# Kernel tuning notes

Hardware: AMD Instinct MI355X
Metric: run time of the kernel (lower is better)

The kernel has to match this reference:

```python
import jax, jax.numpy as jnp
import numpy as np

B, N, D = 2, 2048, 1024
H = 16
D_HEAD = D // H
WINDOW = 128


def setup_inputs() -> dict:
    key = jax.random.key(0)
    ks = jax.random.split(key, 9)
    s = 1.0 / np.sqrt(D)
    return {
        "x": jax.random.normal(ks[0], (B, N, D), dtype=jnp.float32),
        "Wq": jax.random.uniform(ks[1], (D, D), jnp.float32, -s, s),
        "bq": jax.random.uniform(ks[2], (D,), jnp.float32, -s, s),
        "Wk": jax.random.uniform(ks[3], (D, D), jnp.float32, -s, s),
        "bk": jax.random.uniform(ks[4], (D,), jnp.float32, -s, s),
        "Wv": jax.random.uniform(ks[5], (D, D), jnp.float32, -s, s),
        "bv": jax.random.uniform(ks[6], (D,), jnp.float32, -s, s),
        "Wo": jax.random.uniform(ks[7], (D, D), jnp.float32, -s, s),
        "bo": jax.random.uniform(ks[8], (D,), jnp.float32, -s, s),
    }


def reference(x, Wq, bq, Wk, bk, Wv, bv, Wo, bo):
    # Projections (torch Linear: x @ W.T + b), split into heads: (B,H,N,d)
    def proj(W, b):
        y = x @ W.T + b
        return y.reshape(B, N, H, D_HEAD).transpose(0, 2, 1, 3)

    Q = proj(Wq, bq)
    K = proj(Wk, bk)
    V = proj(Wv, bv)

    scale = 1.0 / np.sqrt(D_HEAD)
    scores = jnp.einsum("bhqd,bhkd->bhqk", Q, K) * scale  # (B,H,N,N)

    i = jnp.arange(N)[:, None]
    j = jnp.arange(N)[None, :]
    band = jnp.abs(i - j) <= WINDOW  # (N,N) sliding-window band mask
    scores = jnp.where(band, scores, -jnp.inf)

    probs = jax.nn.softmax(scores, axis=-1)
    out = jnp.einsum("bhqk,bhkd->bhqd", probs, V)  # (B,H,N,d)
    out = out.transpose(0, 2, 1, 3).reshape(B, N, D)
    return out @ Wo.T + bo
```

## Files before the change

kernel.cpp:

```cpp
#include <hip/hip_runtime.h>
#include <hip/hip_bf16.h>
#include <stdint.h>

typedef __bf16 bf16_t;
typedef __bf16 bf16x8 __attribute__((ext_vector_type(8)));
typedef float f32x4 __attribute__((ext_vector_type(4)));

#define NB 2
#define NN 2048
#define ND 1024
#define NH 16
#define DHEAD 64
#define WIN 128

__device__ __forceinline__ void load_lds16(const void* g, void* l) {
  __builtin_amdgcn_global_load_lds(
      (const __attribute__((address_space(1))) uint32_t*)g,
      (__attribute__((address_space(3))) uint32_t*)l, 16, 0, 0);
}

__global__ __launch_bounds__(256)
void cast_all(const float* __restrict__ x,
              const float* __restrict__ Wq, const float* __restrict__ Wk,
              const float* __restrict__ Wv, const float* __restrict__ Wo,
              bf16_t* __restrict__ xb,
              bf16_t* __restrict__ Wqb, bf16_t* __restrict__ Wkb,
              bf16_t* __restrict__ Wvb, bf16_t* __restrict__ Wob) {
  int i = blockIdx.x * 256 + threadIdx.x;
  const float* in;
  bf16_t* out;
  int off;
  if (i < 1048576) {
    in = x; out = xb; off = i;
  } else {
    int j = i - 1048576;
    int wsel = j >> 18;
    off = j & 262143;
    in  = (wsel == 0) ? Wq  : (wsel == 1) ? Wk  : (wsel == 2) ? Wv  : Wo;
    out = (wsel == 0) ? Wqb : (wsel == 1) ? Wkb : (wsel == 2) ? Wvb : Wob;
  }
  float4 v = reinterpret_cast<const float4*>(in)[off];
  union { bf16_t h[4]; uint2 u; } o;
  o.h[0] = (bf16_t)v.x; o.h[1] = (bf16_t)v.y;
  o.h[2] = (bf16_t)v.z; o.h[3] = (bf16_t)v.w;
  reinterpret_cast<uint2*>(out)[off] = o.u;
}

__global__ __launch_bounds__(512, 6)
void qkv_gemm(const bf16_t* __restrict__ xb,
              const bf16_t* __restrict__ Wqb, const bf16_t* __restrict__ Wkb,
              const bf16_t* __restrict__ Wvb,
              const float* __restrict__ bq, const float* __restrict__ bk,
              const float* __restrict__ bv,
              bf16_t* __restrict__ Qh, bf16_t* __restrict__ Kh,
              bf16_t* __restrict__ VTt) {
  __shared__ __align__(16) bf16_t As[2 * 4096];
  __shared__ __align__(16) bf16_t Bs[2 * 4096];

  const int z = blockIdx.z;
  const bf16_t* Bw  = (z == 0) ? Wqb : (z == 1) ? Wkb : Wvb;
  const float* bias = (z == 0) ? bq  : (z == 1) ? bk  : bv;
  const int m0 = blockIdx.y * 128, n0 = blockIdx.x * 128;

  const int tid = threadIdx.x, lane = tid & 63, w = tid >> 6;
  const int wm = w >> 2, wn = w & 3;
  const int lrow = lane & 15, lkg = lane >> 4;
  const int sr = lane >> 2;
  const int sc = ((lane & 3) ^ ((lane >> 3) & 3)) * 8;

  const bf16_t* abase = xb + (size_t)(m0 + w * 16 + sr) * 1024 + sc;
  const bf16_t* bbase = Bw + (size_t)(n0 + w * 16 + sr) * 1024 + sc;

  f32x4 acc[4][2] = {};

  auto stage = [&](int buf, int k0) {
    load_lds16(abase + k0, As + buf * 4096 + w * 512);
    load_lds16(bbase + k0, Bs + buf * 4096 + w * 512);
  };

  stage(0, 0);
  __syncthreads();

  for (int t = 0; t < 32; ++t) {
    if (t < 31) stage((t + 1) & 1, (t + 1) << 5);
    const bf16_t* Ab = As + (t & 1) * 4096;
    const bf16_t* Bb = Bs + (t & 1) * 4096;
    bf16x8 af[4], bf[2];
#pragma unroll
    for (int m = 0; m < 4; ++m) {
      const int row = wm * 64 + m * 16 + lrow;
      af[m] = *reinterpret_cast<const bf16x8*>(Ab + row * 32 + ((lkg ^ ((row >> 1) & 3)) << 3));
    }
#pragma unroll
    for (int n = 0; n < 2; ++n) {
      const int row = wn * 32 + n * 16 + lrow;
      bf[n] = *reinterpret_cast<const bf16x8*>(Bb + row * 32 + ((lkg ^ ((row >> 1) & 3)) << 3));
    }
#pragma unroll
    for (int m = 0; m < 4; ++m)
#pragma unroll
      for (int n = 0; n < 2; ++n)
        acc[m][n] = __builtin_amdgcn_mfma_f32_16x16x32_bf16(af[m], bf[n], acc[m][n], 0, 0, 0);
    __syncthreads();
  }

#pragma unroll
  for (int m = 0; m < 4; ++m)
#pragma unroll
    for (int n = 0; n < 2; ++n)
#pragma unroll
      for (int r = 0; r < 4; ++r) {
        int row = m0 + wm * 64 + m * 16 + lkg * 4 + r;
        int col = n0 + wn * 32 + n * 16 + lrow;
        float val = acc[m][n][r] + bias[col];
        int bb = row >> 11, tok = row & 2047;
        int hh = col >> 6,  dd = col & 63;
        if (z == 2) {
          VTt[((((size_t)(bb * NH + hh) * 32 + (tok >> 6)) * 64 + dd) << 6) + (tok & 63)] = (bf16_t)val;
        } else {
          bf16_t* outp = (z == 0) ? Qh : Kh;
          outp[(((size_t)(bb * NH + hh) * NN + tok) << 6) + dd] = (bf16_t)val;
        }
      }
}

__global__ __launch_bounds__(512, 2)
void out_gemm3(const bf16_t* __restrict__ AOb, const bf16_t* __restrict__ Wob,
               const float* __restrict__ bo, float* __restrict__ Cout) {
  __shared__ __align__(16) bf16_t lds[24576];

  const int m0 = blockIdx.y * 128, n0 = blockIdx.x * 64;
  const int tid = threadIdx.x, lane = tid & 63, w = tid >> 6;
  const int g = w >> 2;
  const int pr = w & 3;
  const int wr = pr >> 1, wc = pr & 1;
  const int lrow = lane & 15, lkg = lane >> 4;
  const int sr = lane >> 2;
  const int sc = ((lane & 3) ^ ((lane >> 3) & 3)) * 8;

  const bf16_t* abase = AOb + (size_t)(m0 + sr) * 1024 + g * 512 + sc;
  const bf16_t* bbase = Wob + (size_t)(n0 + pr * 16 + sr) * 1024 + g * 512 + sc;

  f32x4 acc[4][2] = {};

  auto stage = [&](int buf, int k0) {
    bf16_t* seg = &lds[(g * 2 + buf) * 6144];
#pragma unroll
    for (int i = 0; i < 2; ++i) {
      const int unit = pr * 2 + i;
      load_lds16(abase + (size_t)unit * 16 * 1024 + k0, seg + unit * 512);
    }
    load_lds16(bbase + k0, seg + 4096 + pr * 512);
  };

  stage(0, 0);
  __syncthreads();

  for (int t = 0; t < 16; ++t) {
    if (t < 15) stage((t + 1) & 1, (t + 1) << 5);
    const bf16_t* seg = &lds[(g * 2 + (t & 1)) * 6144];
    const bf16_t* Bb = seg + 4096;
    bf16x8 af[4], bf[2];
#pragma unroll
    for (int m = 0; m < 4; ++m) {
      const int row = wr * 64 + m * 16 + lrow;
      af[m] = *reinterpret_cast<const bf16x8*>(seg + row * 32 + ((lkg ^ ((row >> 1) & 3)) << 3));
    }
#pragma unroll
    for (int n = 0; n < 2; ++n) {
      const int row = wc * 32 + n * 16 + lrow;
      bf[n] = *reinterpret_cast<const bf16x8*>(Bb + row * 32 + ((lkg ^ ((row >> 1) & 3)) << 3));
    }
#pragma unroll
    for (int m = 0; m < 4; ++m)
#pragma unroll
      for (int n = 0; n < 2; ++n)
        acc[m][n] = __builtin_amdgcn_mfma_f32_16x16x32_bf16(af[m], bf[n], acc[m][n], 0, 0, 0);
    __syncthreads();
  }

  float* fl = reinterpret_cast<float*>(lds);
  if (g == 1) {
#pragma unroll
    for (int m = 0; m < 4; ++m)
#pragma unroll
      for (int n = 0; n < 2; ++n)
#pragma unroll
        for (int r = 0; r < 4; ++r)
          fl[pr * 2048 + ((m * 2 + n) * 4 + r) * 64 + lane] = acc[m][n][r];
  }
  __syncthreads();
  if (g == 0) {
#pragma unroll
    for (int m = 0; m < 4; ++m)
#pragma unroll
      for (int n = 0; n < 2; ++n)
#pragma unroll
        for (int r = 0; r < 4; ++r) {
          int row = m0 + wr * 64 + m * 16 + lkg * 4 + r;
          int col = n0 + wc * 32 + n * 16 + lrow;
          float val = acc[m][n][r] + fl[pr * 2048 + ((m * 2 + n) * 4 + r) * 64 + lane] + bo[col];
          Cout[(size_t)row * 1024 + col] = val;
        }
  }
}

__global__ __launch_bounds__(256)
void attn_kernel(const bf16_t* __restrict__ Qh, const bf16_t* __restrict__ Kh,
                 const bf16_t* __restrict__ VTt, bf16_t* __restrict__ AO) {
  __shared__ __align__(16) bf16_t KV_lds[2][2][4096];
  __shared__ uint32_t P_lds[4][16][32];

  const int work = ((blockIdx.x & 7) << 7) | (blockIdx.x >> 3);
  const int qt = work & 31, h = (work >> 5) & 15, b = work >> 9;
  const int tid = threadIdx.x, lane = tid & 63, w = tid >> 6;
  const int lrow = lane & 15, lkg = lane >> 4;
  const int q0 = qt * 64;
  const int qb = q0 + w * 16;
  const int qrow = qb + lrow;
  const int rs7 = lrow & 7;

  const int srow8 = lane >> 3;
  const int sswz  = 8 * ((lane & 7) ^ srow8);

  const bf16_t* kbase = Kh  + (((size_t)(b * NH + h) * NN) << 6);
  const bf16_t* vbase = VTt + ((size_t)(b * NH + h) * 32) * 4096;

  const bf16_t* qptr = Qh + (((size_t)(b * NH + h) * NN + qrow) << 6) + lkg * 8;
  bf16x8 qf0 = *reinterpret_cast<const bf16x8*>(qptr);
  bf16x8 qf1 = *reinterpret_cast<const bf16x8*>(qptr + 32);

  float m_run = -1e30f, l_run = 0.f;
  f32x4 o[4] = {};

  const int kstart = (q0 - WIN > 0) ? (q0 - WIN) : 0;
  const int kend = (q0 + 64 + WIN < NN) ? (q0 + 64 + WIN) : NN;
  const int nch = (kend - kstart) >> 6;
  const float scale = 0.125f;

  auto stage = [&](int bufi, int kc) {
#pragma unroll
    for (int j = 0; j < 2; ++j) {
      const int i = w * 2 + j;
      load_lds16(kbase + (((size_t)(kc + i * 8 + srow8)) << 6) + sswz,
                 &KV_lds[bufi][0][i * 512]);
      load_lds16(vbase + (((size_t)((kc >> 6) * 64 + i * 8 + srow8)) << 6) + sswz,
                 &KV_lds[bufi][1][i * 512]);
    }
  };

  stage(0, kstart);
  __syncthreads();

  for (int ic = 0; ic < nch; ++ic) {
    const int kc = kstart + ic * 64;
    const int bi = ic & 1;
    if (ic + 1 < nch) stage(bi ^ 1, kc + 64);

    const bf16_t* Kt = &KV_lds[bi][0][0];
    const bf16_t* Vt = &KV_lds[bi][1][0];

    f32x4 s[4];
#pragma unroll
    for (int t = 0; t < 4; ++t) {
      const bf16_t* kr = Kt + (t * 16 + lrow) * 64;
      bf16x8 kf0 = *reinterpret_cast<const bf16x8*>(kr + ((lkg ^ rs7) << 3));
      bf16x8 kf1 = *reinterpret_cast<const bf16x8*>(kr + (((4 + lkg) ^ rs7) << 3));
      f32x4 zz = {};
      zz = __builtin_amdgcn_mfma_f32_16x16x32_bf16(kf0, qf0, zz, 0, 0, 0);
      zz = __builtin_amdgcn_mfma_f32_16x16x32_bf16(kf1, qf1, zz, 0, 0, 0);
      s[t] = zz;
    }

    bf16x8 vf0[4], vf1[4];
#pragma unroll
    for (int f = 0; f < 4; ++f) {
      const bf16_t* vr = Vt + (f * 16 + lrow) * 64;
      vf0[f] = *reinterpret_cast<const bf16x8*>(vr + ((lkg ^ rs7) << 3));
      vf1[f] = *reinterpret_cast<const bf16x8*>(vr + (((4 + lkg) ^ rs7) << 3));
    }

    const bool needs_mask = (kc < qb - 113) || (kc > qb + 65);
    float p[4][4];
    float mloc = -1e30f, rsum = 0.f;
    if (needs_mask) {
      float v[4][4];
#pragma unroll
      for (int t = 0; t < 4; ++t)
#pragma unroll
        for (int r = 0; r < 4; ++r) {
          int k = kc + t * 16 + lkg * 4 + r;
          int d = qrow - k;
          bool ok = (unsigned)(d + WIN) <= 2u * WIN;
          v[t][r] = ok ? s[t][r] * scale : -1e30f;
          mloc = fmaxf(mloc, v[t][r]);
        }
      mloc = fmaxf(mloc, __shfl_xor(mloc, 16, 64));
      mloc = fmaxf(mloc, __shfl_xor(mloc, 32, 64));
      float mn = fmaxf(m_run, mloc);
      float corr = __expf(m_run - mn);
      m_run = mn;
#pragma unroll
      for (int t = 0; t < 4; ++t)
#pragma unroll
        for (int r = 0; r < 4; ++r) {
          int k = kc + t * 16 + lkg * 4 + r;
          int d = qrow - k;
          bool ok = (unsigned)(d + WIN) <= 2u * WIN;
          p[t][r] = ok ? __expf(v[t][r] - mn) : 0.f;
          rsum += p[t][r];
        }
      rsum += __shfl_xor(rsum, 16, 64);
      rsum += __shfl_xor(rsum, 32, 64);
      l_run = l_run * corr + rsum;
#pragma unroll
      for (int f = 0; f < 4; ++f) o[f] *= corr;
    } else {
      float v[4][4];
#pragma unroll
      for (int t = 0; t < 4; ++t)
#pragma unroll
        for (int r = 0; r < 4; ++r) {
          v[t][r] = s[t][r] * scale;
          mloc = fmaxf(mloc, v[t][r]);
        }
      mloc = fmaxf(mloc, __shfl_xor(mloc, 16, 64));
      mloc = fmaxf(mloc, __shfl_xor(mloc, 32, 64));
      float mn = fmaxf(m_run, mloc);
      float corr = __expf(m_run - mn);
      m_run = mn;
#pragma unroll
      for (int t = 0; t < 4; ++t)
#pragma unroll
        for (int r = 0; r < 4; ++r) {
          p[t][r] = __expf(v[t][r] - mn);
          rsum += p[t][r];
        }
      rsum += __shfl_xor(rsum, 16, 64);
      rsum += __shfl_xor(rsum, 32, 64);
      l_run = l_run * corr + rsum;
#pragma unroll
      for (int f = 0; f < 4; ++f) o[f] *= corr;
    }

    uint32_t* prow = &P_lds[w][lrow][0];
#pragma unroll
    for (int t = 0; t < 4; ++t)
#pragma unroll
      for (int c = 0; c < 2; ++c) {
        union { bf16_t hh[2]; uint32_t u; } pk;
        pk.hh[0] = (bf16_t)p[t][2 * c];
        pk.hh[1] = (bf16_t)p[t][2 * c + 1];
        int L = 8 * t + 2 * lkg + c;
        int pos = (((L >> 2) ^ rs7) << 2) | (L & 3);
        prow[pos] = pk.u;
      }
    asm volatile("" ::: "memory");
    const bf16_t* prd = reinterpret_cast<const bf16_t*>(&P_lds[w][lrow][0]);
    bf16x8 pa0 = *reinterpret_cast<const bf16x8*>(prd + ((lkg ^ rs7) << 3));
    bf16x8 pa1 = *reinterpret_cast<const bf16x8*>(prd + (((4 + lkg) ^ rs7) << 3));

#pragma unroll
    for (int f = 0; f < 4; ++f) {
      o[f] = __builtin_amdgcn_mfma_f32_16x16x32_bf16(vf0[f], pa0, o[f], 0, 0, 0);
      o[f] = __builtin_amdgcn_mfma_f32_16x16x32_bf16(vf1[f], pa1, o[f], 0, 0, 0);
    }
    __syncthreads();
  }

  float inv = 1.0f / l_run;
#pragma unroll
  for (int f = 0; f < 4; ++f) {
    union { bf16_t hh[4]; uint2 u; } ov;
#pragma unroll
    for (int r = 0; r < 4; ++r) ov.hh[r] = (bf16_t)(o[f][r] * inv);
    bf16_t* op = AO + (size_t)(b * NN + qrow) * ND + h * DHEAD + f * 16 + lkg * 4;
    *reinterpret_cast<uint2*>(op) = ov.u;
  }
}

extern "C" void kernel_launch(void* const* d_in, const int* in_sizes, int n_in,
                              void* d_out, int out_size, void* d_ws, size_t ws_size,
                              hipStream_t stream) {
  const float* x  = (const float*)d_in[0];
  const float* Wq = (const float*)d_in[1];
  const float* bq = (const float*)d_in[2];
  const float* Wk = (const float*)d_in[3];
  const float* bk = (const float*)d_in[4];
  const float* Wv = (const float*)d_in[5];
  const float* bv = (const float*)d_in[6];
  const float* Wo = (const float*)d_in[7];
  const float* bo = (const float*)d_in[8];
  float* out = (float*)d_out;

  bf16_t* ws  = (bf16_t*)d_ws;
  bf16_t* xb  = ws;
  bf16_t* Wqb = xb  + 4194304;
  bf16_t* Wkb = Wqb + 1048576;
  bf16_t* Wvb = Wkb + 1048576;
  bf16_t* Wob = Wvb + 1048576;
  bf16_t* Qh  = Wob + 1048576;
  bf16_t* Kh  = Qh  + 4194304;
  bf16_t* VTt = Kh  + 4194304;
  bf16_t* AOb = VTt + 4194304;

  cast_all<<<8192, 256, 0, stream>>>(x, Wq, Wk, Wv, Wo, xb, Wqb, Wkb, Wvb, Wob);

  qkv_gemm<<<dim3(8, 32, 3), 512, 0, stream>>>(xb, Wqb, Wkb, Wvb, bq, bk, bv, Qh, Kh, VTt);
  attn_kernel<<<1024, 256, 0, stream>>>(Qh, Kh, VTt, AOb);
  out_gemm3<<<dim3(16, 32), 512, 0, stream>>>(AOb, Wob, bo, out);
}
```

Measured before the change: 91.29 us.

## Enlarge QKV GEMM tiles to 256x256 with triple-buffered LDS pipeline

Reworks the QKV projection GEMM from 128x128 tiles with a double buffer to 256x256 tiles with a three-stage LDS ring. A and B loads for step t+2 are interleaved between two MFMA half-phases, using explicit waitcnt, barriers and setprio. The launch becomes a 1D grid of 192 blocks with a swizzled block-to-tile mapping to improve L2 reuse. Each thread carries more accumulators and occupancy drops to 2 waves per SIMD. With only 192 blocks on the device, some CUs may be left underused.

```diff
diff --git a/kernel.cpp b/kernel.cpp
--- a/kernel.cpp
+++ b/kernel.cpp
@@ -46,7 +46,7 @@
   reinterpret_cast<uint2*>(out)[off] = o.u;
 }
 
-__global__ __launch_bounds__(512, 6)
+__global__ __launch_bounds__(512, 2)
 void qkv_gemm(const bf16_t* __restrict__ xb,
               const bf16_t* __restrict__ Wqb, const bf16_t* __restrict__ Wkb,
               const bf16_t* __restrict__ Wvb,
@@ -54,13 +54,16 @@
               const float* __restrict__ bv,
               bf16_t* __restrict__ Qh, bf16_t* __restrict__ Kh,
               bf16_t* __restrict__ VTt) {
-  __shared__ __align__(16) bf16_t As[2 * 4096];
-  __shared__ __align__(16) bf16_t Bs[2 * 4096];
-
-  const int z = blockIdx.z;
+  __shared__ __align__(16) bf16_t lds[3][16384];
+
+  const int raw = blockIdx.x;
+  const int swz = (raw & 7) * 24 + (raw >> 3);
+  const int mt = swz / 12, nt = swz % 12;
+  const int m0 = mt * 256;
+  const int z = nt >> 2;
+  const int n0z = (nt & 3) * 256;
   const bf16_t* Bw  = (z == 0) ? Wqb : (z == 1) ? Wkb : Wvb;
   const float* bias = (z == 0) ? bq  : (z == 1) ? bk  : bv;
-  const int m0 = blockIdx.y * 128, n0 = blockIdx.x * 128;
 
   const int tid = threadIdx.x, lane = tid & 63, w = tid >> 6;
   const int wm = w >> 2, wn = w & 3;
@@ -68,53 +71,97 @@
   const int sr = lane >> 2;
   const int sc = ((lane & 3) ^ ((lane >> 3) & 3)) * 8;
 
-  const bf16_t* abase = xb + (size_t)(m0 + w * 16 + sr) * 1024 + sc;
-  const bf16_t* bbase = Bw + (size_t)(n0 + w * 16 + sr) * 1024 + sc;
-
-  f32x4 acc[4][2] = {};
-
-  auto stage = [&](int buf, int k0) {
-    load_lds16(abase + k0, As + buf * 4096 + w * 512);
-    load_lds16(bbase + k0, Bs + buf * 4096 + w * 512);
+  const bf16_t* asrc = xb + (size_t)(m0 + w * 16 + sr) * 1024 + sc;
+  const bf16_t* bsrc = Bw + (size_t)(n0z + w * 16 + sr) * 1024 + sc;
+
+  f32x4 acc[8][4] = {};
+
+  auto stageA = [&](int t) {
+    bf16_t* buf = &lds[t % 3][0];
+    const int k0 = t << 5;
+    load_lds16(asrc + k0,          buf + w * 512);
+    load_lds16(asrc + 131072 + k0, buf + 4096 + w * 512);
   };
-
-  stage(0, 0);
-  __syncthreads();
+  auto stageB = [&](int t) {
+    bf16_t* buf = &lds[t % 3][0];
+    const int k0 = t << 5;
+    load_lds16(bsrc + k0,          buf + 8192 + w * 512);
+    load_lds16(bsrc + 131072 + k0, buf + 12288 + w * 512);
+  };
+
+  stageA(0); stageB(0); stageA(1); stageB(1);
+  asm volatile("s_waitcnt vmcnt(4)" ::: "memory");
+  __builtin_amdgcn_s_barrier();
+  asm volatile("" ::: "memory");
 
   for (int t = 0; t < 32; ++t) {
-    if (t < 31) stage((t + 1) & 1, (t + 1) << 5);
-    const bf16_t* Ab = As + (t & 1) * 4096;
-    const bf16_t* Bb = Bs + (t & 1) * 4096;
-    bf16x8 af[4], bf[2];
+    const bf16_t* A = &lds[t % 3][0];
+    const bf16_t* B = A + 8192;
+    bf16x8 bfr[4], af[4];
+
+#pragma unroll
+    for (int n = 0; n < 4; ++n) {
+      const int row = wn * 64 + n * 16 + lrow;
+      bfr[n] = *reinterpret_cast<const bf16x8*>(B + row * 32 + ((lkg ^ ((row >> 1) & 3)) << 3));
+    }
 #pragma unroll
     for (int m = 0; m < 4; ++m) {
-      const int row = wm * 64 + m * 16 + lrow;
-      af[m] = *reinterpret_cast<const bf16x8*>(Ab + row * 32 + ((lkg ^ ((row >> 1) & 3)) << 3));
-    }
-#pragma unroll
-    for (int n = 0; n < 2; ++n) {
-      const int row = wn * 32 + n * 16 + lrow;
-      bf[n] = *reinterpret_cast<const bf16x8*>(Bb + row * 32 + ((lkg ^ ((row >> 1) & 3)) << 3));
-    }
+      const int row = wm * 128 + m * 16 + lrow;
+      af[m] = *reinterpret_cast<const bf16x8*>(A + row * 32 + ((lkg ^ ((row >> 1) & 3)) << 3));
+    }
+    if (t + 2 < 32) stageA(t + 2);
+    asm volatile("" ::: "memory");
+    __builtin_amdgcn_s_barrier();
+    asm volatile("s_waitcnt lgkmcnt(0)" ::: "memory");
+    __builtin_amdgcn_sched_barrier(0);
+    __builtin_amdgcn_s_setprio(1);
 #pragma unroll
     for (int m = 0; m < 4; ++m)
 #pragma unroll
-      for (int n = 0; n < 2; ++n)
-        acc[m][n] = __builtin_amdgcn_mfma_f32_16x16x32_bf16(af[m], bf[n], acc[m][n], 0, 0, 0);
-    __syncthreads();
-  }
-
-#pragma unroll
-  for (int m = 0; m < 4; ++m)
-#pragma unroll
-    for (int n = 0; n < 2; ++n)
+      for (int n = 0; n < 4; ++n)
+        acc[m][n] = __builtin_amdgcn_mfma_f32_16x16x32_bf16(af[m], bfr[n], acc[m][n], 0, 0, 0);
+    __builtin_amdgcn_s_setprio(0);
+    asm volatile("" ::: "memory");
+    __builtin_amdgcn_s_barrier();
+    asm volatile("" ::: "memory");
+
+#pragma unroll
+    for (int m = 0; m < 4; ++m) {
+      const int row = wm * 128 + (4 + m) * 16 + lrow;
+      af[m] = *reinterpret_cast<const bf16x8*>(A + row * 32 + ((lkg ^ ((row >> 1) & 3)) << 3));
+    }
+    if (t + 2 < 32) stageB(t + 2);
+    asm volatile("" ::: "memory");
+    __builtin_amdgcn_s_barrier();
+    asm volatile("s_waitcnt lgkmcnt(0)" ::: "memory");
+    __builtin_amdgcn_sched_barrier(0);
+    __builtin_amdgcn_s_setprio(1);
+#pragma unroll
+    for (int m = 0; m < 4; ++m)
+#pragma unroll
+      for (int n = 0; n < 4; ++n)
+        acc[4 + m][n] = __builtin_amdgcn_mfma_f32_16x16x32_bf16(af[m], bfr[n], acc[4 + m][n], 0, 0, 0);
+    __builtin_amdgcn_s_setprio(0);
+    if (t < 30) {
+      asm volatile("s_waitcnt vmcnt(4)" ::: "memory");
+    } else {
+      asm volatile("s_waitcnt vmcnt(0)" ::: "memory");
+    }
+    __builtin_amdgcn_s_barrier();
+    asm volatile("" ::: "memory");
+  }
+
+#pragma unroll
+  for (int m = 0; m < 8; ++m)
+#pragma unroll
+    for (int n = 0; n < 4; ++n)
 #pragma unroll
       for (int r = 0; r < 4; ++r) {
-        int row = m0 + wm * 64 + m * 16 + lkg * 4 + r;
-        int col = n0 + wn * 32 + n * 16 + lrow;
+        const int row = m0 + wm * 128 + m * 16 + lkg * 4 + r;
+        const int col = n0z + wn * 64 + n * 16 + lrow;
         float val = acc[m][n][r] + bias[col];
-        int bb = row >> 11, tok = row & 2047;
-        int hh = col >> 6,  dd = col & 63;
+        const int bb = row >> 11, tok = row & 2047;
+        const int hh = col >> 6, dd = col & 63;
         if (z == 2) {
           VTt[((((size_t)(bb * NH + hh) * 32 + (tok >> 6)) * 64 + dd) << 6) + (tok & 63)] = (bf16_t)val;
         } else {
@@ -406,7 +453,7 @@
 
   cast_all<<<8192, 256, 0, stream>>>(x, Wq, Wk, Wv, Wo, xb, Wqb, Wkb, Wvb, Wob);
 
-  qkv_gemm<<<dim3(8, 32, 3), 512, 0, stream>>>(xb, Wqb, Wkb, Wvb, bq, bk, bv, Qh, Kh, VTt);
+  qkv_gemm<<<192, 512, 0, stream>>>(xb, Wqb, Wkb, Wvb, bq, bk, bv, Qh, Kh, VTt);
   attn_kernel<<<1024, 256, 0, stream>>>(Qh, Kh, VTt, AOb);
   out_gemm3<<<dim3(16, 32), 512, 0, stream>>>(AOb, Wob, bo, out);
 }
```

After: 112.1 us. +22.8%, slower.

## Retile QKV GEMM over concatenated weights and drop split-K in output GEMM

Applied to the files above, without the earlier changes.

The QKV projection now treats Wq/Wk/Wv as one contiguous 3072-column weight (relying on the adjacent workspace layout). It uses 128x96 tiles with 6 waves and a 1D swizzled grid of 1024 blocks, which makes the block count a multiple of the CU count. The output GEMM drops the two-group split-K with its LDS reduction in favour of plain 64x64 tiles with 4 waves and a swizzled 1024-block grid. The aim is better wave balance and L2 locality, at the cost of per-column bias selection and smaller tiles with less operand reuse in the output GEMM.

```diff
diff --git a/kernel.cpp b/kernel.cpp
--- a/kernel.cpp
+++ b/kernel.cpp
@@ -46,36 +46,37 @@
   reinterpret_cast<uint2*>(out)[off] = o.u;
 }
 
-__global__ __launch_bounds__(512, 6)
+__global__ __launch_bounds__(384, 6)
 void qkv_gemm(const bf16_t* __restrict__ xb,
-              const bf16_t* __restrict__ Wqb, const bf16_t* __restrict__ Wkb,
-              const bf16_t* __restrict__ Wvb,
+              const bf16_t* __restrict__ Wcat,
               const float* __restrict__ bq, const float* __restrict__ bk,
               const float* __restrict__ bv,
               bf16_t* __restrict__ Qh, bf16_t* __restrict__ Kh,
               bf16_t* __restrict__ VTt) {
-  __shared__ __align__(16) bf16_t As[2 * 4096];
-  __shared__ __align__(16) bf16_t Bs[2 * 4096];
-
-  const int z = blockIdx.z;
-  const bf16_t* Bw  = (z == 0) ? Wqb : (z == 1) ? Wkb : Wvb;
-  const float* bias = (z == 0) ? bq  : (z == 1) ? bk  : bv;
-  const int m0 = blockIdx.y * 128, n0 = blockIdx.x * 128;
+  __shared__ __align__(16) bf16_t lds[2 * 7168];
+
+  const int raw = blockIdx.x;
+  const int swz = (raw & 7) * 128 + (raw >> 3);
+  const int mt = swz >> 5, ntt = swz & 31;
+  const int m0 = mt * 128, n0 = ntt * 96;
 
   const int tid = threadIdx.x, lane = tid & 63, w = tid >> 6;
-  const int wm = w >> 2, wn = w & 3;
+  const int wm = w / 3, wn = w % 3;
   const int lrow = lane & 15, lkg = lane >> 4;
   const int sr = lane >> 2;
   const int sc = ((lane & 3) ^ ((lane >> 3) & 3)) * 8;
 
-  const bf16_t* abase = xb + (size_t)(m0 + w * 16 + sr) * 1024 + sc;
-  const bf16_t* bbase = Bw + (size_t)(n0 + w * 16 + sr) * 1024 + sc;
+  const bf16_t* asrc = xb   + (size_t)(m0 + sr) * 1024 + sc;
+  const bf16_t* bsrc = Wcat + (size_t)(n0 + sr) * 1024 + sc;
 
   f32x4 acc[4][2] = {};
 
   auto stage = [&](int buf, int k0) {
-    load_lds16(abase + k0, As + buf * 4096 + w * 512);
-    load_lds16(bbase + k0, Bs + buf * 4096 + w * 512);
+    bf16_t* base = lds + buf * 7168;
+    load_lds16(asrc + (size_t)w * 16384 + k0, base + w * 512);
+    load_lds16(bsrc + (size_t)w * 16384 + k0, base + 4096 + w * 512);
+    if (w < 2)
+      load_lds16(asrc + (size_t)(6 + w) * 16384 + k0, base + (6 + w) * 512);
   };
 
   stage(0, 0);
@@ -83,8 +84,8 @@
 
   for (int t = 0; t < 32; ++t) {
     if (t < 31) stage((t + 1) & 1, (t + 1) << 5);
-    const bf16_t* Ab = As + (t & 1) * 4096;
-    const bf16_t* Bb = Bs + (t & 1) * 4096;
+    const bf16_t* Ab = lds + (t & 1) * 7168;
+    const bf16_t* Bb = Ab + 4096;
     bf16x8 af[4], bf[2];
 #pragma unroll
     for (int m = 0; m < 4; ++m) {
@@ -110,61 +111,61 @@
     for (int n = 0; n < 2; ++n)
 #pragma unroll
       for (int r = 0; r < 4; ++r) {
-        int row = m0 + wm * 64 + m * 16 + lkg * 4 + r;
-        int col = n0 + wn * 32 + n * 16 + lrow;
-        float val = acc[m][n][r] + bias[col];
-        int bb = row >> 11, tok = row & 2047;
-        int hh = col >> 6,  dd = col & 63;
-        if (z == 2) {
+        const int row = m0 + wm * 64 + m * 16 + lkg * 4 + r;
+        const int col = n0 + wn * 32 + n * 16 + lrow;
+        const int zz = col >> 10, c = col & 1023;
+        float bval = (zz == 0) ? bq[c] : (zz == 1) ? bk[c] : bv[c];
+        float val = acc[m][n][r] + bval;
+        const int bb = row >> 11, tok = row & 2047;
+        const int hh = c >> 6, dd = c & 63;
+        if (zz == 2) {
           VTt[((((size_t)(bb * NH + hh) * 32 + (tok >> 6)) * 64 + dd) << 6) + (tok & 63)] = (bf16_t)val;
         } else {
-          bf16_t* outp = (z == 0) ? Qh : Kh;
+          bf16_t* outp = (zz == 0) ? Qh : Kh;
           outp[(((size_t)(bb * NH + hh) * NN + tok) << 6) + dd] = (bf16_t)val;
         }
       }
 }
 
-__global__ __launch_bounds__(512, 2)
-void out_gemm3(const bf16_t* __restrict__ AOb, const bf16_t* __restrict__ Wob,
+__global__ __launch_bounds__(256, 4)
+void out_gemm4(const bf16_t* __restrict__ AOb, const bf16_t* __restrict__ Wob,
                const float* __restrict__ bo, float* __restrict__ Cout) {
-  __shared__ __align__(16) bf16_t lds[24576];
-
-  const int m0 = blockIdx.y * 128, n0 = blockIdx.x * 64;
+  __shared__ __align__(16) bf16_t lds[2 * 4096];
+
+  const int raw = blockIdx.x;
+  const int swz = (raw & 7) * 128 + (raw >> 3);
+  const int mt = swz >> 4, ntt = swz & 15;
+  const int m0 = mt * 64, n0 = ntt * 64;
+
   const int tid = threadIdx.x, lane = tid & 63, w = tid >> 6;
-  const int g = w >> 2;
-  const int pr = w & 3;
-  const int wr = pr >> 1, wc = pr & 1;
+  const int wr = w >> 1, wc = w & 1;
   const int lrow = lane & 15, lkg = lane >> 4;
   const int sr = lane >> 2;
   const int sc = ((lane & 3) ^ ((lane >> 3) & 3)) * 8;
 
-  const bf16_t* abase = AOb + (size_t)(m0 + sr) * 1024 + g * 512 + sc;
-  const bf16_t* bbase = Wob + (size_t)(n0 + pr * 16 + sr) * 1024 + g * 512 + sc;
-
-  f32x4 acc[4][2] = {};
+  const bf16_t* abase = AOb + (size_t)(m0 + sr) * 1024 + sc;
+  const bf16_t* bbase = Wob + (size_t)(n0 + sr) * 1024 + sc;
+
+  f32x4 acc[2][2] = {};
 
   auto stage = [&](int buf, int k0) {
-    bf16_t* seg = &lds[(g * 2 + buf) * 6144];
-#pragma unroll
-    for (int i = 0; i < 2; ++i) {
-      const int unit = pr * 2 + i;
-      load_lds16(abase + (size_t)unit * 16 * 1024 + k0, seg + unit * 512);
-    }
-    load_lds16(bbase + k0, seg + 4096 + pr * 512);
+    bf16_t* base = lds + buf * 4096;
+    load_lds16(abase + (size_t)w * 16384 + k0, base + w * 512);
+    load_lds16(bbase + (size_t)w * 16384 + k0, base + 2048 + w * 512);
   };
 
   stage(0, 0);
   __syncthreads();
 
-  for (int t = 0; t < 16; ++t) {
-    if (t < 15) stage((t + 1) & 1, (t + 1) << 5);
-    const bf16_t* seg = &lds[(g * 2 + (t & 1)) * 6144];
-    const bf16_t* Bb = seg + 4096;
-    bf16x8 af[4], bf[2];
-#pragma unroll
-    for (int m = 0; m < 4; ++m) {
-      const int row = wr * 64 + m * 16 + lrow;
-      af[m] = *reinterpret_cast<const bf16x8*>(seg + row * 32 + ((lkg ^ ((row >> 1) & 3)) << 3));
+  for (int t = 0; t < 32; ++t) {
+    if (t < 31) stage((t + 1) & 1, (t + 1) << 5);
+    const bf16_t* Ab = lds + (t & 1) * 4096;
+    const bf16_t* Bb = Ab + 2048;
+    bf16x8 af[2], bf[2];
+#pragma unroll
+    for (int m = 0; m < 2; ++m) {
+      const int row = wr * 32 + m * 16 + lrow;
+      af[m] = *reinterpret_cast<const bf16x8*>(Ab + row * 32 + ((lkg ^ ((row >> 1) & 3)) << 3));
     }
 #pragma unroll
     for (int n = 0; n < 2; ++n) {
@@ -172,37 +173,23 @@
       bf[n] = *reinterpret_cast<const bf16x8*>(Bb + row * 32 + ((lkg ^ ((row >> 1) & 3)) << 3));
     }
 #pragma unroll
-    for (int m = 0; m < 4; ++m)
+    for (int m = 0; m < 2; ++m)
 #pragma unroll
       for (int n = 0; n < 2; ++n)
         acc[m][n] = __builtin_amdgcn_mfma_f32_16x16x32_bf16(af[m], bf[n], acc[m][n], 0, 0, 0);
     __syncthreads();
   }
 
-  float* fl = reinterpret_cast<float*>(lds);
-  if (g == 1) {
-#pragma unroll
-    for (int m = 0; m < 4; ++m)
-#pragma unroll
-      for (int n = 0; n < 2; ++n)
-#pragma unroll
-        for (int r = 0; r < 4; ++r)
-          fl[pr * 2048 + ((m * 2 + n) * 4 + r) * 64 + lane] = acc[m][n][r];
-  }
-  __syncthreads();
-  if (g == 0) {
-#pragma unroll
-    for (int m = 0; m < 4; ++m)
-#pragma unroll
-      for (int n = 0; n < 2; ++n)
-#pragma unroll
-        for (int r = 0; r < 4; ++r) {
-          int row = m0 + wr * 64 + m * 16 + lkg * 4 + r;
-          int col = n0 + wc * 32 + n * 16 + lrow;
-          float val = acc[m][n][r] + fl[pr * 2048 + ((m * 2 + n) * 4 + r) * 64 + lane] + bo[col];
-          Cout[(size_t)row * 1024 + col] = val;
-        }
-  }
+#pragma unroll
+  for (int m = 0; m < 2; ++m)
+#pragma unroll
+    for (int n = 0; n < 2; ++n)
+#pragma unroll
+      for (int r = 0; r < 4; ++r) {
+        int row = m0 + wr * 32 + m * 16 + lkg * 4 + r;
+        int col = n0 + wc * 32 + n * 16 + lrow;
+        Cout[(size_t)row * 1024 + col] = acc[m][n][r] + bo[col];
+      }
 }
 
 __global__ __launch_bounds__(256)
@@ -406,7 +393,7 @@
 
   cast_all<<<8192, 256, 0, stream>>>(x, Wq, Wk, Wv, Wo, xb, Wqb, Wkb, Wvb, Wob);
 
-  qkv_gemm<<<dim3(8, 32, 3), 512, 0, stream>>>(xb, Wqb, Wkb, Wvb, bq, bk, bv, Qh, Kh, VTt);
+  qkv_gemm<<<1024, 384, 0, stream>>>(xb, Wqb, bq, bk, bv, Qh, Kh, VTt);
   attn_kernel<<<1024, 256, 0, stream>>>(Qh, Kh, VTt, AOb);
-  out_gemm3<<<dim3(16, 32), 512, 0, stream>>>(AOb, Wob, bo, out);
-}
+  out_gemm4<<<1024, 256, 0, stream>>>(AOb, Wob, bo, out);
+}
```

Result: slower. 101.9 us (+11.6%).
